# Kernel tuning notes

Hardware: AMD Instinct MI355X
Metric: run time of the kernel (lower is better)

The kernel has to match this reference:

```python
import jax, jax.numpy as jnp
import numpy as np
from jax import lax

DN = ('NCHW', 'OIHW', 'NCHW')

def conv(x, w, b, stride):
    y = lax.conv_general_dilated(x, w, window_strides=(stride, stride),
                                 padding='VALID', dimension_numbers=DN)
    return y + b[None, :, None, None]

def setup_inputs() -> dict:
    key = jax.random.key(0)
    ks = jax.random.split(key, 7)
    B = 4096
    def he(k, shape, fan_in):
        return jax.random.normal(k, shape, jnp.float32) * np.sqrt(2.0 / fan_in)
    return {
        'x':  jax.random.normal(ks[0], (B, 3, 48, 64), jnp.float32),
        'w1': he(ks[1], (32, 3, 8, 8), 3 * 8 * 8),
        'b1': jnp.zeros((32,), jnp.float32),
        'w2': he(ks[2], (64, 32, 3, 3), 32 * 3 * 3),
        'b2': jnp.zeros((64,), jnp.float32),
        'w3': he(ks[3], (64, 64, 3, 3), 64 * 3 * 3),
        'b3': jnp.zeros((64,), jnp.float32),
        'w4': he(ks[4], (512, 960), 960),
        'b4': jnp.zeros((512,), jnp.float32),
        'w5': he(ks[5], (2, 512), 512),
        'b5': jnp.zeros((2,), jnp.float32),
    }

def reference(x, w1, b1, w2, b2, w3, b3, w4, b4, w5, b5):
    # conv1 (k8 s4): [B,3,48,64] -> [B,32,11,15]
    x1 = conv(x, w1, b1, 4)
    # side reduction (torch code does this on CPU with python loops):
    # sum over batch and channel dims of pre-ReLU activation, divided by 32
    ave1 = jnp.sum(x1, axis=(0, 1)) / 32.0          # [11,15]
    x2 = jax.nn.relu(x1)
    # conv2 (k3 s2): -> [B,64,5,7]
    x3 = conv(x2, w2, b2, 2)
    ave2 = jnp.sum(x3, axis=(0, 1)) / 64.0          # [5,7]
    x4 = jax.nn.relu(x3)
    # conv3 (k3 s1): -> [B,64,3,5]
    x5 = conv(x4, w3, b3, 1)
    ave3 = jnp.sum(x5, axis=(0, 1)) / 64.0          # [3,5]
    x6 = jax.nn.relu(x5)
    # fc head: flatten (C,H,W order, matching torch) -> 960 -> 512 -> 2
    h = x6.reshape(x6.shape[0], -1)                 # [B,960]
    h = jax.nn.relu(h @ w4.T + b4)
    out = h @ w5.T + b5                             # [B,2]
    return out, ave1, ave2, ave3
```

## Files before the change

kernel.cpp:

```cpp
#include <hip/hip_runtime.h>
#include <hip/hip_bf16.h>

#define BATCH 4096

typedef __attribute__((ext_vector_type(8))) short short8;
typedef __attribute__((ext_vector_type(4))) short short4_t;
typedef __attribute__((ext_vector_type(4))) float f32x4;

#define MFMA_BF16 __builtin_amdgcn_mfma_f32_16x16x32_bf16

__device__ __forceinline__ float frelu(float v) { return v > 0.f ? v : 0.f; }
__device__ __forceinline__ unsigned short f2bf(float f) {
    return __builtin_bit_cast(unsigned short, __float2bfloat16(f));
}
__device__ __forceinline__ short8 cvt8(const float* p) {
    float4 a = *(const float4*)p;
    float4 b = *(const float4*)(p + 4);
    short8 r;
    r[0] = (short)f2bf(a.x); r[1] = (short)f2bf(a.y); r[2] = (short)f2bf(a.z); r[3] = (short)f2bf(a.w);
    r[4] = (short)f2bf(b.x); r[5] = (short)f2bf(b.y); r[6] = (short)f2bf(b.z); r[7] = (short)f2bf(b.w);
    return r;
}

__global__ __launch_bounds__(256) void prep_kernel(const float* __restrict__ w2, const float* __restrict__ w3,
                                                   const float* __restrict__ w4, const float* __restrict__ b5,
                                                   unsigned short* __restrict__ w2p, unsigned short* __restrict__ w3p,
                                                   unsigned short* __restrict__ w4p, float* __restrict__ out) {
    int idx = blockIdx.x * 256 + threadIdx.x;
    if (idx < 18432) {
        int oc = idx / 288, k = idx % 288;
        int khw = k / 32, ic = k % 32;
        w2p[idx] = f2bf(w2[oc * 288 + ic * 9 + khw]);
    } else if (idx < 55296) {
        int j = idx - 18432;
        int oc = j / 576, k = j % 576;
        int khw = k / 64, ic = k % 64;
        w3p[j] = f2bf(w3[oc * 576 + ic * 9 + khw]);
    } else if (idx < 546816) {
        int j = idx - 55296;
        int n = j / 960, k = j % 960;
        int pos = k / 64, oc = k % 64;
        w4p[j] = f2bf(w4[n * 960 + oc * 15 + pos]);
    } else if (idx < 555008) {
        int j = idx - 546816;
        out[j] = b5[j & 1];
    } else if (idx < 555223) {
        out[8192 + (idx - 555008)] = 0.f;
    }
}

__global__ __launch_bounds__(256) void conv1_mfma(const float* __restrict__ x,
                                                  const float* __restrict__ w1, const float* __restrict__ b1,
                                                  unsigned short* __restrict__ x2, float* __restrict__ red1) {
    constexpr int RS = 68;
    __shared__ __align__(16) unsigned short xl[3 * 48 * RS];
    __shared__ __align__(16) unsigned short ol[165 * 32];
    __shared__ float red[176];
    const int img = blockIdx.x;
    const int tid = threadIdx.x;
    const int wave = tid >> 6, lane = tid & 63;
    const int col = lane & 15, quad = lane >> 4;
    if (tid < 176) red[tid] = 0.f;

    {
        const float4* xs = (const float4*)(x + (size_t)img * 9216);
        #pragma unroll
        for (int i = 0; i < 9; ++i) {
            const int idx = tid + i * 256;
            float4 v = xs[idx];
            const int fo = idx * 4;
            const int r = fo >> 6;
            const int cf = fo & 63;
            short4_t s;
            s[0] = (short)f2bf(v.x); s[1] = (short)f2bf(v.y);
            s[2] = (short)f2bf(v.z); s[3] = (short)f2bf(v.w);
            *(short4_t*)(xl + r * RS + cf) = s;
        }
    }

    short8 Bf[2][6];
    #pragma unroll
    for (int nt = 0; nt < 2; ++nt) {
        const int oc = nt * 16 + col;
        #pragma unroll
        for (int c = 0; c < 6; ++c)
            Bf[nt][c] = cvt8(w1 + oc * 192 + c * 32 + quad * 8);
    }
    const float bias0 = b1[col], bias1 = b1[col + 16];
    __syncthreads();

    #pragma unroll
    for (int ti = 0; ti < 3; ++ti) {
        const int t = wave + ti * 4;
        if (t >= 11) break;
        const int posA = t * 16 + col;
        const int pm = posA < 165 ? posA : 164;
        const int oh = pm / 15, ow = pm % 15;
        f32x4 acc0 = {0.f, 0.f, 0.f, 0.f}, acc1 = {0.f, 0.f, 0.f, 0.f};
        #pragma unroll
        for (int c = 0; c < 6; ++c) {
            const int ic = c >> 1;
            const int kh = (c & 1) * 4 + quad;
            const unsigned short* ap = xl + (ic * 48 + oh * 4 + kh) * RS + ow * 4;
            short8 af;
            *(short4_t*)&af       = *(const short4_t*)ap;
            *((short4_t*)&af + 1) = *(const short4_t*)(ap + 4);
            acc0 = MFMA_BF16(af, Bf[0][c], acc0, 0, 0, 0);
            acc1 = MFMA_BF16(af, Bf[1][c], acc1, 0, 0, 0);
        }
        #pragma unroll
        for (int r = 0; r < 4; ++r) {
            const int pr = t * 16 + quad * 4 + r;
            float v0 = acc0[r] + bias0;
            float v1 = acc1[r] + bias1;
            float s = v0 + v1;
            s += __shfl_xor(s, 1); s += __shfl_xor(s, 2);
            s += __shfl_xor(s, 4); s += __shfl_xor(s, 8);
            if (pr < 165) {
                if (col == 0) atomicAdd(&red[pr], s);
                ol[pr * 32 + col]      = f2bf(frelu(v0));
                ol[pr * 32 + col + 16] = f2bf(frelu(v1));
            }
        }
    }
    __syncthreads();
    {
        float4* dst = (float4*)(x2 + (size_t)img * 5280);
        const float4* src = (const float4*)ol;
        for (int i = tid; i < 660; i += 256) dst[i] = src[i];
    }
    if (tid < 176) red1[(size_t)tid * 4096 + img] = red[tid];
}

__global__ __launch_bounds__(256) void reduce1_kernel(const float* __restrict__ red1, float* __restrict__ ave1) {
    const int pos = blockIdx.x;
    float s = 0.f;
    for (int i = threadIdx.x; i < 4096; i += 256) s += red1[(size_t)pos * 4096 + i];
    s += __shfl_down(s, 32); s += __shfl_down(s, 16); s += __shfl_down(s, 8);
    s += __shfl_down(s, 4);  s += __shfl_down(s, 2);  s += __shfl_down(s, 1);
    __shared__ float wsum[4];
    if ((threadIdx.x & 63) == 0) wsum[threadIdx.x >> 6] = s;
    __syncthreads();
    if (threadIdx.x == 0) ave1[pos] = (wsum[0] + wsum[1] + wsum[2] + wsum[3]) * 0.03125f;
}

__global__ __launch_bounds__(256) void conv2_mfma(const unsigned short* __restrict__ x2,
                                                  const unsigned short* __restrict__ w2p, const float* __restrict__ b2,
                                                  unsigned short* __restrict__ x4, float* __restrict__ ave2) {
    __shared__ unsigned short wl[64 * 296];
    __shared__ float red[35];
    const int tid = threadIdx.x;
    {
        const float4* src = (const float4*)w2p;
        for (int i = tid; i < 2304; i += 256) {
            int row = i / 36, off = i % 36;
            *(float4*)((char*)wl + row * 592 + off * 16) = src[i];
        }
    }
    if (tid < 35) red[tid] = 0.f;
    __syncthreads();

    const int wave = tid >> 6, lane = tid & 63;
    const int col = lane & 15, quad = lane >> 4;
    const int tile0 = blockIdx.x * 16 + wave * 4;

    const unsigned short* abase[4];
    #pragma unroll
    for (int mi = 0; mi < 4; ++mi) {
        const int m = (tile0 + mi) * 16 + col;
        const int b = m / 35, pos = m % 35;
        const int oh = pos / 7, ow = pos % 7;
        abase[mi] = x2 + ((size_t)b * 165 + oh * 30 + ow * 2) * 32 + quad * 8;
    }
    f32x4 acc[4][4] = {};
    #pragma unroll
    for (int c = 0; c < 9; ++c) {
        const int kh = c / 3, kw = c % 3;
        short8 Bf[4];
        #pragma unroll
        for (int nt = 0; nt < 4; ++nt)
            Bf[nt] = *(const short8*)((const char*)wl + ((nt * 16 + col) * 296 + c * 32 + quad * 8) * 2);
        #pragma unroll
        for (int mi = 0; mi < 4; ++mi) {
            short8 af = *(const short8*)(abase[mi] + (kh * 15 + kw) * 32);
            #pragma unroll
            for (int nt = 0; nt < 4; ++nt)
                acc[mi][nt] = MFMA_BF16(af, Bf[nt], acc[mi][nt], 0, 0, 0);
        }
    }
    float bv[4];
    #pragma unroll
    for (int nt = 0; nt < 4; ++nt) bv[nt] = b2[nt * 16 + col];
    #pragma unroll
    for (int mi = 0; mi < 4; ++mi) {
        const int mrow0 = (tile0 + mi) * 16;
        #pragma unroll
        for (int r = 0; r < 4; ++r) {
            const int m = mrow0 + quad * 4 + r;
            const int b = m / 35, pos = m % 35;
            unsigned short* dst = x4 + ((size_t)b * 35 + pos) * 64;
            float s = 0.f;
            #pragma unroll
            for (int nt = 0; nt < 4; ++nt) {
                float v = acc[mi][nt][r] + bv[nt];
                s += v;
                dst[nt * 16 + col] = f2bf(frelu(v));
            }
            s += __shfl_xor(s, 1); s += __shfl_xor(s, 2); s += __shfl_xor(s, 4); s += __shfl_xor(s, 8);
            if (col == 0) atomicAdd(&red[pos], s);
        }
    }
    __syncthreads();
    if (tid < 35) atomicAdd(&ave2[tid], red[tid] * 0.015625f);
}

__global__ __launch_bounds__(256) void conv3_mfma(const unsigned short* __restrict__ x4,
                                                  const unsigned short* __restrict__ w3p, const float* __restrict__ b3,
                                                  unsigned short* __restrict__ x6, float* __restrict__ ave3) {
    __shared__ unsigned short wl[32 * 584];
    __shared__ float red[15];
    const int tid = threadIdx.x;
    const int oc0 = blockIdx.y * 32;
    {
        const float4* src = (const float4*)(w3p + (size_t)oc0 * 576);
        for (int i = tid; i < 2304; i += 256) {
            int row = i / 72, off = i % 72;
            *(float4*)((char*)wl + row * 1168 + off * 16) = src[i];
        }
    }
    if (tid < 15) red[tid] = 0.f;
    __syncthreads();

    const int wave = tid >> 6, lane = tid & 63;
    const int col = lane & 15, quad = lane >> 4;
    const int tile0 = blockIdx.x * 16 + wave * 4;

    const unsigned short* abase[4];
    #pragma unroll
    for (int mi = 0; mi < 4; ++mi) {
        const int m = (tile0 + mi) * 16 + col;
        const int b = m / 15, pos = m % 15;
        const int oh = pos / 5, ow = pos % 5;
        abase[mi] = x4 + ((size_t)b * 35 + oh * 7 + ow) * 64 + quad * 8;
    }
    f32x4 acc[4][2] = {};
    #pragma unroll
    for (int c = 0; c < 18; ++c) {
        const int khw = c >> 1, kh = khw / 3, kw = khw % 3;
        const int icoff = (c & 1) * 32;
        short8 Bf[2];
        #pragma unroll
        for (int nt = 0; nt < 2; ++nt)
            Bf[nt] = *(const short8*)((const char*)wl + ((nt * 16 + col) * 584 + c * 32 + quad * 8) * 2);
        #pragma unroll
        for (int mi = 0; mi < 4; ++mi) {
            short8 af = *(const short8*)(abase[mi] + (kh * 7 + kw) * 64 + icoff);
            #pragma unroll
            for (int nt = 0; nt < 2; ++nt)
                acc[mi][nt] = MFMA_BF16(af, Bf[nt], acc[mi][nt], 0, 0, 0);
        }
    }
    float bv[2];
    #pragma unroll
    for (int nt = 0; nt < 2; ++nt) bv[nt] = b3[oc0 + nt * 16 + col];
    #pragma unroll
    for (int mi = 0; mi < 4; ++mi) {
        const int mrow0 = (tile0 + mi) * 16;
        #pragma unroll
        for (int r = 0; r < 4; ++r) {
            const int m = mrow0 + quad * 4 + r;
            const int b = m / 15, pos = m % 15;
            unsigned short* dst = x6 + (size_t)b * 960 + pos * 64 + oc0;
            float s = 0.f;
            #pragma unroll
            for (int nt = 0; nt < 2; ++nt) {
                float v = acc[mi][nt][r] + bv[nt];
                s += v;
                dst[nt * 16 + col] = f2bf(frelu(v));
            }
            s += __shfl_xor(s, 1); s += __shfl_xor(s, 2); s += __shfl_xor(s, 4); s += __shfl_xor(s, 8);
            if (col == 0) atomicAdd(&red[pos], s);
        }
    }
    __syncthreads();
    if (tid < 15) atomicAdd(&ave3[tid], red[tid] * 0.015625f);
}

__global__ __launch_bounds__(256) void fc4_mfma(const unsigned short* __restrict__ x6,
                                                const unsigned short* __restrict__ w4p, const float* __restrict__ b4,
                                                const float* __restrict__ w5, float* __restrict__ out) {
    const int tid = threadIdx.x;
    const int wave = tid >> 6, lane = tid & 63;
    const int col = lane & 15, quad = lane >> 4;
    const int m0 = blockIdx.x * 128 + wave * 32;
    const int n0 = blockIdx.y * 64;

    const unsigned short* arow0 = x6 + (size_t)(m0 + col) * 960 + quad * 8;
    const unsigned short* arow1 = arow0 + 16 * 960;
    f32x4 acc[2][4] = {};
    for (int c = 0; c < 30; ++c) {
        short8 Bf[4];
        #pragma unroll
        for (int nt = 0; nt < 4; ++nt)
            Bf[nt] = *(const short8*)(w4p + (size_t)(n0 + nt * 16 + col) * 960 + c * 32 + quad * 8);
        short8 a0 = *(const short8*)(arow0 + c * 32);
        short8 a1 = *(const short8*)(arow1 + c * 32);
        #pragma unroll
        for (int nt = 0; nt < 4; ++nt) {
            acc[0][nt] = MFMA_BF16(a0, Bf[nt], acc[0][nt], 0, 0, 0);
            acc[1][nt] = MFMA_BF16(a1, Bf[nt], acc[1][nt], 0, 0, 0);
        }
    }
    float bv[4], w50[4], w51[4];
    #pragma unroll
    for (int nt = 0; nt < 4; ++nt) {
        const int oc = n0 + nt * 16 + col;
        bv[nt] = b4[oc]; w50[nt] = w5[oc]; w51[nt] = w5[512 + oc];
    }
    #pragma unroll
    for (int mi = 0; mi < 2; ++mi) {
        #pragma unroll
        for (int r = 0; r < 4; ++r) {
            float l0 = 0.f, l1 = 0.f;
            #pragma unroll
            for (int nt = 0; nt < 4; ++nt) {
                float hh = frelu(acc[mi][nt][r] + bv[nt]);
                l0 += hh * w50[nt];
                l1 += hh * w51[nt];
            }
            l0 += __shfl_xor(l0, 1); l0 += __shfl_xor(l0, 2); l0 += __shfl_xor(l0, 4); l0 += __shfl_xor(l0, 8);
            l1 += __shfl_xor(l1, 1); l1 += __shfl_xor(l1, 2); l1 += __shfl_xor(l1, 4); l1 += __shfl_xor(l1, 8);
            if (col == 0) {
                const int gm = m0 + mi * 16 + quad * 4 + r;
                atomicAdd(&out[gm * 2 + 0], l0);
                atomicAdd(&out[gm * 2 + 1], l1);
            }
        }
    }
}

extern "C" void kernel_launch(void* const* d_in, const int* in_sizes, int n_in,
                              void* d_out, int out_size, void* d_ws, size_t ws_size,
                              hipStream_t stream) {
    const float* x  = (const float*)d_in[0];
    const float* w1 = (const float*)d_in[1];
    const float* b1 = (const float*)d_in[2];
    const float* w2 = (const float*)d_in[3];
    const float* b2 = (const float*)d_in[4];
    const float* w3 = (const float*)d_in[5];
    const float* b3 = (const float*)d_in[6];
    const float* w4 = (const float*)d_in[7];
    const float* b4 = (const float*)d_in[8];
    const float* w5 = (const float*)d_in[9];
    const float* b5 = (const float*)d_in[10];
    float* out = (float*)d_out;

    unsigned short* ws = (unsigned short*)d_ws;
    unsigned short* x2  = ws;
    unsigned short* x4  = ws + 21626880;
    unsigned short* x6  = ws + 30801920;
    unsigned short* w2p = ws + 34734080;
    unsigned short* w3p = ws + 34752512;
    unsigned short* w4p = ws + 34789376;
    float* red1 = (float*)((char*)d_ws + 70561792);

    float* ave1 = out + 8192;
    float* ave2 = out + 8192 + 165;
    float* ave3 = out + 8192 + 200;

    prep_kernel<<<2169, 256, 0, stream>>>(w2, w3, w4, b5, w2p, w3p, w4p, out);
    conv1_mfma<<<BATCH, 256, 0, stream>>>(x, w1, b1, x2, red1);
    reduce1_kernel<<<165, 256, 0, stream>>>(red1, ave1);
    conv2_mfma<<<560, 256, 0, stream>>>(x2, w2p, b2, x4, ave2);
    conv3_mfma<<<dim3(240, 2), 256, 0, stream>>>(x4, w3p, b3, x6, ave3);
    fc4_mfma<<<dim3(32, 8), 256, 0, stream>>>(x6, w4p, b4, w5, out);
}
```

Measured before the change: 345.0 us.

## Fuse conv1-conv3 per image in LDS and retile fc head

Merges the three conv kernels into one per-image kernel that keeps the conv1 and conv2 activations in shared memory, so the x2 and x4 intermediates no longer make a round trip through global memory. The three spatial-sum reductions become one batched reduce kernel. The fc kernel moves to smaller M tiles (32 rows, one N tile per wave) and accumulates its output in shared memory before global atomics. In exchange, each block now loads the conv2 and conv3 weights straight from global memory into registers, which adds register pressure and redundant weight traffic per image.

```diff
diff --git a/kernel.cpp b/kernel.cpp
--- a/kernel.cpp
+++ b/kernel.cpp
@@ -49,18 +49,28 @@
     }
 }
 
-__global__ __launch_bounds__(256) void conv1_mfma(const float* __restrict__ x,
-                                                  const float* __restrict__ w1, const float* __restrict__ b1,
-                                                  unsigned short* __restrict__ x2, float* __restrict__ red1) {
+__global__ __launch_bounds__(256) void fused_convs(const float* __restrict__ x,
+                                                   const float* __restrict__ w1, const float* __restrict__ b1,
+                                                   const unsigned short* __restrict__ w2p, const float* __restrict__ b2,
+                                                   const unsigned short* __restrict__ w3p, const float* __restrict__ b3,
+                                                   unsigned short* __restrict__ x6, float* __restrict__ redbuf) {
     constexpr int RS = 68;
     __shared__ __align__(16) unsigned short xl[3 * 48 * RS];
-    __shared__ __align__(16) unsigned short ol[165 * 32];
-    __shared__ float red[176];
+    __shared__ __align__(16) unsigned short x2l[165 * 36];
+    __shared__ float red1l[165];
+    __shared__ float red2l[35];
+    __shared__ float red3l[15];
+    unsigned short* x4l = xl;
+    unsigned short* x6l = xl + 2560;
+
     const int img = blockIdx.x;
     const int tid = threadIdx.x;
     const int wave = tid >> 6, lane = tid & 63;
     const int col = lane & 15, quad = lane >> 4;
-    if (tid < 176) red[tid] = 0.f;
+
+    if (tid < 165) red1l[tid] = 0.f;
+    else if (tid < 200) red2l[tid - 165] = 0.f;
+    else if (tid < 215) red3l[tid - 200] = 0.f;
 
     {
         const float4* xs = (const float4*)(x + (size_t)img * 9216);
@@ -69,8 +79,7 @@
             const int idx = tid + i * 256;
             float4 v = xs[idx];
             const int fo = idx * 4;
-            const int r = fo >> 6;
-            const int cf = fo & 63;
+            const int r = fo >> 6, cf = fo & 63;
             short4_t s;
             s[0] = (short)f2bf(v.x); s[1] = (short)f2bf(v.y);
             s[2] = (short)f2bf(v.z); s[3] = (short)f2bf(v.w);
@@ -78,13 +87,13 @@
         }
     }
 
-    short8 Bf[2][6];
+    short8 Bf1[2][6];
     #pragma unroll
     for (int nt = 0; nt < 2; ++nt) {
         const int oc = nt * 16 + col;
         #pragma unroll
         for (int c = 0; c < 6; ++c)
-            Bf[nt][c] = cvt8(w1 + oc * 192 + c * 32 + quad * 8);
+            Bf1[nt][c] = cvt8(w1 + oc * 192 + c * 32 + quad * 8);
     }
     const float bias0 = b1[col], bias1 = b1[col + 16];
     __syncthreads();
@@ -105,8 +114,8 @@
             short8 af;
             *(short4_t*)&af       = *(const short4_t*)ap;
             *((short4_t*)&af + 1) = *(const short4_t*)(ap + 4);
-            acc0 = MFMA_BF16(af, Bf[0][c], acc0, 0, 0, 0);
-            acc1 = MFMA_BF16(af, Bf[1][c], acc1, 0, 0, 0);
+            acc0 = MFMA_BF16(af, Bf1[0][c], acc0, 0, 0, 0);
+            acc1 = MFMA_BF16(af, Bf1[1][c], acc1, 0, 0, 0);
         }
         #pragma unroll
         for (int r = 0; r < 4; ++r) {
@@ -117,226 +126,156 @@
             s += __shfl_xor(s, 1); s += __shfl_xor(s, 2);
             s += __shfl_xor(s, 4); s += __shfl_xor(s, 8);
             if (pr < 165) {
-                if (col == 0) atomicAdd(&red[pr], s);
-                ol[pr * 32 + col]      = f2bf(frelu(v0));
-                ol[pr * 32 + col + 16] = f2bf(frelu(v1));
-            }
-        }
-    }
-    __syncthreads();
+                if (col == 0) atomicAdd(&red1l[pr], s);
+                x2l[pr * 36 + col]      = f2bf(frelu(v0));
+                x2l[pr * 36 + col + 16] = f2bf(frelu(v1));
+            }
+        }
+    }
+    __syncthreads();
+
     {
-        float4* dst = (float4*)(x2 + (size_t)img * 5280);
-        const float4* src = (const float4*)ol;
-        for (int i = tid; i < 660; i += 256) dst[i] = src[i];
-    }
-    if (tid < 176) red1[(size_t)tid * 4096 + img] = red[tid];
-}
-
-__global__ __launch_bounds__(256) void reduce1_kernel(const float* __restrict__ red1, float* __restrict__ ave1) {
-    const int pos = blockIdx.x;
+        const int oc2 = wave * 16 + col;
+        short8 Bf2[9];
+        #pragma unroll
+        for (int c = 0; c < 9; ++c)
+            Bf2[c] = *(const short8*)(w2p + (size_t)oc2 * 288 + c * 32 + quad * 8);
+        const float bv2 = b2[oc2];
+
+        int aoff[3];
+        #pragma unroll
+        for (int mt = 0; mt < 3; ++mt) {
+            int p = mt * 16 + col; p = p < 35 ? p : 34;
+            const int oh2 = p / 7, ow2 = p % 7;
+            aoff[mt] = (oh2 * 30 + ow2 * 2) * 36 + quad * 8;
+        }
+        f32x4 acc[3] = {};
+        #pragma unroll
+        for (int c = 0; c < 9; ++c) {
+            const int kh = c / 3, kw = c % 3;
+            const int koff = (kh * 15 + kw) * 36;
+            #pragma unroll
+            for (int mt = 0; mt < 3; ++mt) {
+                const unsigned short* ap = x2l + aoff[mt] + koff;
+                short8 af;
+                *(short4_t*)&af       = *(const short4_t*)ap;
+                *((short4_t*)&af + 1) = *(const short4_t*)(ap + 4);
+                acc[mt] = MFMA_BF16(af, Bf2[c], acc[mt], 0, 0, 0);
+            }
+        }
+        #pragma unroll
+        for (int mt = 0; mt < 3; ++mt) {
+            #pragma unroll
+            for (int r = 0; r < 4; ++r) {
+                const int pr = mt * 16 + quad * 4 + r;
+                float v = acc[mt][r] + bv2;
+                float s = v;
+                s += __shfl_xor(s, 1); s += __shfl_xor(s, 2);
+                s += __shfl_xor(s, 4); s += __shfl_xor(s, 8);
+                if (pr < 35) {
+                    x4l[pr * 72 + oc2] = f2bf(frelu(v));
+                    if (col == 0) atomicAdd(&red2l[pr], s);
+                }
+            }
+        }
+    }
+    __syncthreads();
+
+    {
+        const int oc3 = wave * 16 + col;
+        short8 Bf3[18];
+        #pragma unroll
+        for (int c = 0; c < 18; ++c)
+            Bf3[c] = *(const short8*)(w3p + (size_t)oc3 * 576 + c * 32 + quad * 8);
+        const float bv3 = b3[oc3];
+
+        int p = col < 15 ? col : 14;
+        const int abase = ((p / 5) * 7 + (p % 5)) * 72;
+        f32x4 acc = {};
+        #pragma unroll
+        for (int c = 0; c < 18; ++c) {
+            const int khw = c >> 1, kh = khw / 3, kw = khw % 3;
+            const unsigned short* ap = x4l + abase + (kh * 7 + kw) * 72 + (c & 1) * 32 + quad * 8;
+            short8 af = *(const short8*)ap;
+            acc = MFMA_BF16(af, Bf3[c], acc, 0, 0, 0);
+        }
+        #pragma unroll
+        for (int r = 0; r < 4; ++r) {
+            const int pr = quad * 4 + r;
+            float v = acc[r] + bv3;
+            float s = v;
+            s += __shfl_xor(s, 1); s += __shfl_xor(s, 2);
+            s += __shfl_xor(s, 4); s += __shfl_xor(s, 8);
+            if (pr < 15) {
+                x6l[pr * 64 + oc3] = f2bf(frelu(v));
+                if (col == 0) atomicAdd(&red3l[pr], s);
+            }
+        }
+    }
+    __syncthreads();
+
+    if (tid < 120) ((float4*)(x6 + (size_t)img * 960))[tid] = ((const float4*)x6l)[tid];
+    if (tid < 215) {
+        float v = tid < 165 ? red1l[tid] : (tid < 200 ? red2l[tid - 165] : red3l[tid - 200]);
+        redbuf[(size_t)tid * 4096 + img] = v;
+    }
+}
+
+__global__ __launch_bounds__(256) void reduce_aves(const float* __restrict__ redbuf, float* __restrict__ out) {
+    const int row = blockIdx.x;
     float s = 0.f;
-    for (int i = threadIdx.x; i < 4096; i += 256) s += red1[(size_t)pos * 4096 + i];
+    for (int i = threadIdx.x; i < 4096; i += 256) s += redbuf[(size_t)row * 4096 + i];
     s += __shfl_down(s, 32); s += __shfl_down(s, 16); s += __shfl_down(s, 8);
     s += __shfl_down(s, 4);  s += __shfl_down(s, 2);  s += __shfl_down(s, 1);
     __shared__ float wsum[4];
     if ((threadIdx.x & 63) == 0) wsum[threadIdx.x >> 6] = s;
     __syncthreads();
-    if (threadIdx.x == 0) ave1[pos] = (wsum[0] + wsum[1] + wsum[2] + wsum[3]) * 0.03125f;
-}
-
-__global__ __launch_bounds__(256) void conv2_mfma(const unsigned short* __restrict__ x2,
-                                                  const unsigned short* __restrict__ w2p, const float* __restrict__ b2,
-                                                  unsigned short* __restrict__ x4, float* __restrict__ ave2) {
-    __shared__ unsigned short wl[64 * 296];
-    __shared__ float red[35];
-    const int tid = threadIdx.x;
-    {
-        const float4* src = (const float4*)w2p;
-        for (int i = tid; i < 2304; i += 256) {
-            int row = i / 36, off = i % 36;
-            *(float4*)((char*)wl + row * 592 + off * 16) = src[i];
-        }
-    }
-    if (tid < 35) red[tid] = 0.f;
-    __syncthreads();
-
-    const int wave = tid >> 6, lane = tid & 63;
-    const int col = lane & 15, quad = lane >> 4;
-    const int tile0 = blockIdx.x * 16 + wave * 4;
-
-    const unsigned short* abase[4];
-    #pragma unroll
-    for (int mi = 0; mi < 4; ++mi) {
-        const int m = (tile0 + mi) * 16 + col;
-        const int b = m / 35, pos = m % 35;
-        const int oh = pos / 7, ow = pos % 7;
-        abase[mi] = x2 + ((size_t)b * 165 + oh * 30 + ow * 2) * 32 + quad * 8;
-    }
-    f32x4 acc[4][4] = {};
-    #pragma unroll
-    for (int c = 0; c < 9; ++c) {
-        const int kh = c / 3, kw = c % 3;
-        short8 Bf[4];
-        #pragma unroll
-        for (int nt = 0; nt < 4; ++nt)
-            Bf[nt] = *(const short8*)((const char*)wl + ((nt * 16 + col) * 296 + c * 32 + quad * 8) * 2);
-        #pragma unroll
-        for (int mi = 0; mi < 4; ++mi) {
-            short8 af = *(const short8*)(abase[mi] + (kh * 15 + kw) * 32);
-            #pragma unroll
-            for (int nt = 0; nt < 4; ++nt)
-                acc[mi][nt] = MFMA_BF16(af, Bf[nt], acc[mi][nt], 0, 0, 0);
-        }
-    }
-    float bv[4];
-    #pragma unroll
-    for (int nt = 0; nt < 4; ++nt) bv[nt] = b2[nt * 16 + col];
-    #pragma unroll
-    for (int mi = 0; mi < 4; ++mi) {
-        const int mrow0 = (tile0 + mi) * 16;
-        #pragma unroll
-        for (int r = 0; r < 4; ++r) {
-            const int m = mrow0 + quad * 4 + r;
-            const int b = m / 35, pos = m % 35;
-            unsigned short* dst = x4 + ((size_t)b * 35 + pos) * 64;
-            float s = 0.f;
-            #pragma unroll
-            for (int nt = 0; nt < 4; ++nt) {
-                float v = acc[mi][nt][r] + bv[nt];
-                s += v;
-                dst[nt * 16 + col] = f2bf(frelu(v));
-            }
-            s += __shfl_xor(s, 1); s += __shfl_xor(s, 2); s += __shfl_xor(s, 4); s += __shfl_xor(s, 8);
-            if (col == 0) atomicAdd(&red[pos], s);
-        }
-    }
-    __syncthreads();
-    if (tid < 35) atomicAdd(&ave2[tid], red[tid] * 0.015625f);
-}
-
-__global__ __launch_bounds__(256) void conv3_mfma(const unsigned short* __restrict__ x4,
-                                                  const unsigned short* __restrict__ w3p, const float* __restrict__ b3,
-                                                  unsigned short* __restrict__ x6, float* __restrict__ ave3) {
-    __shared__ unsigned short wl[32 * 584];
-    __shared__ float red[15];
-    const int tid = threadIdx.x;
-    const int oc0 = blockIdx.y * 32;
-    {
-        const float4* src = (const float4*)(w3p + (size_t)oc0 * 576);
-        for (int i = tid; i < 2304; i += 256) {
-            int row = i / 72, off = i % 72;
-            *(float4*)((char*)wl + row * 1168 + off * 16) = src[i];
-        }
-    }
-    if (tid < 15) red[tid] = 0.f;
-    __syncthreads();
-
-    const int wave = tid >> 6, lane = tid & 63;
-    const int col = lane & 15, quad = lane >> 4;
-    const int tile0 = blockIdx.x * 16 + wave * 4;
-
-    const unsigned short* abase[4];
-    #pragma unroll
-    for (int mi = 0; mi < 4; ++mi) {
-        const int m = (tile0 + mi) * 16 + col;
-        const int b = m / 15, pos = m % 15;
-        const int oh = pos / 5, ow = pos % 5;
-        abase[mi] = x4 + ((size_t)b * 35 + oh * 7 + ow) * 64 + quad * 8;
-    }
-    f32x4 acc[4][2] = {};
-    #pragma unroll
-    for (int c = 0; c < 18; ++c) {
-        const int khw = c >> 1, kh = khw / 3, kw = khw % 3;
-        const int icoff = (c & 1) * 32;
-        short8 Bf[2];
-        #pragma unroll
-        for (int nt = 0; nt < 2; ++nt)
-            Bf[nt] = *(const short8*)((const char*)wl + ((nt * 16 + col) * 584 + c * 32 + quad * 8) * 2);
-        #pragma unroll
-        for (int mi = 0; mi < 4; ++mi) {
-            short8 af = *(const short8*)(abase[mi] + (kh * 7 + kw) * 64 + icoff);
-            #pragma unroll
-            for (int nt = 0; nt < 2; ++nt)
-                acc[mi][nt] = MFMA_BF16(af, Bf[nt], acc[mi][nt], 0, 0, 0);
-        }
-    }
-    float bv[2];
-    #pragma unroll
-    for (int nt = 0; nt < 2; ++nt) bv[nt] = b3[oc0 + nt * 16 + col];
-    #pragma unroll
-    for (int mi = 0; mi < 4; ++mi) {
-        const int mrow0 = (tile0 + mi) * 16;
-        #pragma unroll
-        for (int r = 0; r < 4; ++r) {
-            const int m = mrow0 + quad * 4 + r;
-            const int b = m / 15, pos = m % 15;
-            unsigned short* dst = x6 + (size_t)b * 960 + pos * 64 + oc0;
-            float s = 0.f;
-            #pragma unroll
-            for (int nt = 0; nt < 2; ++nt) {
-                float v = acc[mi][nt][r] + bv[nt];
-                s += v;
-                dst[nt * 16 + col] = f2bf(frelu(v));
-            }
-            s += __shfl_xor(s, 1); s += __shfl_xor(s, 2); s += __shfl_xor(s, 4); s += __shfl_xor(s, 8);
-            if (col == 0) atomicAdd(&red[pos], s);
-        }
-    }
-    __syncthreads();
-    if (tid < 15) atomicAdd(&ave3[tid], red[tid] * 0.015625f);
-}
-
-__global__ __launch_bounds__(256) void fc4_mfma(const unsigned short* __restrict__ x6,
-                                                const unsigned short* __restrict__ w4p, const float* __restrict__ b4,
-                                                const float* __restrict__ w5, float* __restrict__ out) {
+    if (threadIdx.x == 0)
+        out[8192 + row] = (wsum[0] + wsum[1] + wsum[2] + wsum[3]) * (row < 165 ? 0.03125f : 0.015625f);
+}
+
+__global__ __launch_bounds__(256) void fc45_mfma(const unsigned short* __restrict__ x6,
+                                                 const unsigned short* __restrict__ w4p, const float* __restrict__ b4,
+                                                 const float* __restrict__ w5, float* __restrict__ out) {
+    __shared__ float outl[32][2];
     const int tid = threadIdx.x;
     const int wave = tid >> 6, lane = tid & 63;
     const int col = lane & 15, quad = lane >> 4;
-    const int m0 = blockIdx.x * 128 + wave * 32;
-    const int n0 = blockIdx.y * 64;
-
+    if (tid < 64) outl[tid >> 1][tid & 1] = 0.f;
+    const int m0 = blockIdx.x * 32;
+    const int oc = blockIdx.y * 64 + wave * 16 + col;
+
+    const unsigned short* brow  = w4p + (size_t)oc * 960 + quad * 8;
     const unsigned short* arow0 = x6 + (size_t)(m0 + col) * 960 + quad * 8;
     const unsigned short* arow1 = arow0 + 16 * 960;
-    f32x4 acc[2][4] = {};
+    f32x4 acc0 = {}, acc1 = {};
+    __syncthreads();
+    #pragma unroll 6
     for (int c = 0; c < 30; ++c) {
-        short8 Bf[4];
-        #pragma unroll
-        for (int nt = 0; nt < 4; ++nt)
-            Bf[nt] = *(const short8*)(w4p + (size_t)(n0 + nt * 16 + col) * 960 + c * 32 + quad * 8);
+        short8 Bf = *(const short8*)(brow + c * 32);
         short8 a0 = *(const short8*)(arow0 + c * 32);
         short8 a1 = *(const short8*)(arow1 + c * 32);
-        #pragma unroll
-        for (int nt = 0; nt < 4; ++nt) {
-            acc[0][nt] = MFMA_BF16(a0, Bf[nt], acc[0][nt], 0, 0, 0);
-            acc[1][nt] = MFMA_BF16(a1, Bf[nt], acc[1][nt], 0, 0, 0);
-        }
-    }
-    float bv[4], w50[4], w51[4];
-    #pragma unroll
-    for (int nt = 0; nt < 4; ++nt) {
-        const int oc = n0 + nt * 16 + col;
-        bv[nt] = b4[oc]; w50[nt] = w5[oc]; w51[nt] = w5[512 + oc];
-    }
+        acc0 = MFMA_BF16(a0, Bf, acc0, 0, 0, 0);
+        acc1 = MFMA_BF16(a1, Bf, acc1, 0, 0, 0);
+    }
+    const float bb = b4[oc], u0 = w5[oc], u1 = w5[512 + oc];
     #pragma unroll
     for (int mi = 0; mi < 2; ++mi) {
+        const f32x4 acc = mi ? acc1 : acc0;
         #pragma unroll
         for (int r = 0; r < 4; ++r) {
-            float l0 = 0.f, l1 = 0.f;
-            #pragma unroll
-            for (int nt = 0; nt < 4; ++nt) {
-                float hh = frelu(acc[mi][nt][r] + bv[nt]);
-                l0 += hh * w50[nt];
-                l1 += hh * w51[nt];
-            }
+            float h = frelu(acc[r] + bb);
+            float l0 = h * u0, l1 = h * u1;
             l0 += __shfl_xor(l0, 1); l0 += __shfl_xor(l0, 2); l0 += __shfl_xor(l0, 4); l0 += __shfl_xor(l0, 8);
             l1 += __shfl_xor(l1, 1); l1 += __shfl_xor(l1, 2); l1 += __shfl_xor(l1, 4); l1 += __shfl_xor(l1, 8);
             if (col == 0) {
-                const int gm = m0 + mi * 16 + quad * 4 + r;
-                atomicAdd(&out[gm * 2 + 0], l0);
-                atomicAdd(&out[gm * 2 + 1], l1);
-            }
-        }
-    }
+                atomicAdd(&outl[mi * 16 + quad * 4 + r][0], l0);
+                atomicAdd(&outl[mi * 16 + quad * 4 + r][1], l1);
+            }
+        }
+    }
+    __syncthreads();
+    if (tid < 64) atomicAdd(&out[(m0 + (tid >> 1)) * 2 + (tid & 1)], outl[tid >> 1][tid & 1]);
 }
 
 extern "C" void kernel_launch(void* const* d_in, const int* in_sizes, int n_in,
@@ -356,22 +295,14 @@
     float* out = (float*)d_out;
 
     unsigned short* ws = (unsigned short*)d_ws;
-    unsigned short* x2  = ws;
-    unsigned short* x4  = ws + 21626880;
-    unsigned short* x6  = ws + 30801920;
-    unsigned short* w2p = ws + 34734080;
-    unsigned short* w3p = ws + 34752512;
-    unsigned short* w4p = ws + 34789376;
-    float* red1 = (float*)((char*)d_ws + 70561792);
-
-    float* ave1 = out + 8192;
-    float* ave2 = out + 8192 + 165;
-    float* ave3 = out + 8192 + 200;
+    unsigned short* x6  = ws;
+    unsigned short* w2p = ws + 3932160;
+    unsigned short* w3p = ws + 3950592;
+    unsigned short* w4p = ws + 3987456;
+    float* redbuf = (float*)((char*)d_ws + 8957952);
 
     prep_kernel<<<2169, 256, 0, stream>>>(w2, w3, w4, b5, w2p, w3p, w4p, out);
-    conv1_mfma<<<BATCH, 256, 0, stream>>>(x, w1, b1, x2, red1);
-    reduce1_kernel<<<165, 256, 0, stream>>>(red1, ave1);
-    conv2_mfma<<<560, 256, 0, stream>>>(x2, w2p, b2, x4, ave2);
-    conv3_mfma<<<dim3(240, 2), 256, 0, stream>>>(x4, w3p, b3, x6, ave3);
-    fc4_mfma<<<dim3(32, 8), 256, 0, stream>>>(x6, w4p, b4, w5, out);
-}
+    fused_convs<<<BATCH, 256, 0, stream>>>(x, w1, b1, w2p, b2, w3p, b3, x6, redbuf);
+    reduce_aves<<<215, 256, 0, stream>>>(redbuf, out);
+    fc45_mfma<<<dim3(128, 8), 256, 0, stream>>>(x6, w4p, b4, w5, out);
+}
```

Result: no change. 347.5 us (+0.7%).
